# Kernel optimization log

Hardware: AMD Instinct MI355X
Metric: run time of the kernel (lower is better)

The kernel has to match this reference:

```python
import jax, jax.numpy as jnp
import numpy as np

B, T, IN_DIM = 32, 1024, 32
E, H, P = 256, 4, 32  # embed_dim, heads, max_patches
HD = E // H


def _lin(x, w, b):
    # torch nn.Linear: y = x @ W.T + b, W: [out, in]
    return jnp.einsum('...i,oi->...o', x, w) + b


def setup_inputs() -> dict:
    key = jax.random.key(0)
    ks = jax.random.split(key, 13)
    s = 0.02
    return {
        'x': jax.random.normal(ks[0], (B, T, IN_DIM), jnp.float32),
        'ip_w': jax.random.normal(ks[1], (E, IN_DIM), jnp.float32) * s,
        'ip_b': jnp.zeros((E,), jnp.float32),
        'in_proj_w': jax.random.normal(ks[2], (3 * E, E), jnp.float32) * s,
        'in_proj_b': jnp.zeros((3 * E,), jnp.float32),
        'out_w': jax.random.normal(ks[3], (E, E), jnp.float32) * s,
        'out_b': jnp.zeros((E,), jnp.float32),
        'bp_w1': jax.random.normal(ks[4], (32, E), jnp.float32) * s,
        'bp_b1': jnp.zeros((32,), jnp.float32),
        'bp_w2': jax.random.normal(ks[5], (1, 32), jnp.float32) * s,
        'bp_b2': jnp.zeros((1,), jnp.float32),
        'pr_w': jax.random.normal(ks[6], (E, E), jnp.float32) * s,
        'pr_b': jnp.zeros((E,), jnp.float32),
    }


def reference(x, ip_w, ip_b, in_proj_w, in_proj_b, out_w, out_b,
              bp_w1, bp_b1, bp_w2, bp_b2, pr_w, pr_b):
    # input projection
    h = _lin(x, ip_w, ip_b)  # [B,T,E]
    # MultiheadAttention (self-attn, batch_first, eval/no-dropout)
    qkv = _lin(h, in_proj_w, in_proj_b)  # [B,T,3E]
    q, k, v = jnp.split(qkv, 3, axis=-1)
    q = q.reshape(B, T, H, HD)
    k = k.reshape(B, T, H, HD)
    v = v.reshape(B, T, H, HD)
    scores = jnp.einsum('bqhd,bkhd->bhqk', q, k) / jnp.sqrt(jnp.float32(HD))
    attn = jax.nn.softmax(scores, axis=-1)
    ctx = jnp.einsum('bhqk,bkhd->bqhd', attn, v).reshape(B, T, E)
    attn_out = _lin(ctx, out_w, out_b)  # [B,T,E]
    # boundary scores
    bscore = jax.nn.sigmoid(_lin(jax.nn.relu(_lin(attn_out, bp_w1, bp_b1)), bp_w2, bp_b2))[..., 0]  # [B,T]
    cbp = jnp.cumsum(bscore, axis=1)
    cbp = cbp / (cbp[:, -1:] + 1e-6)
    pid = jnp.minimum(jnp.floor(cbp * P).astype(jnp.int32), P - 1)  # [B,T]
    # segment-mean pooling via scatter-add
    b_idx = jnp.broadcast_to(jnp.arange(B)[:, None], (B, T))
    pe = jnp.zeros((B, P, E), attn_out.dtype).at[b_idx, pid].add(attn_out)
    cnt = jnp.zeros((B, P), attn_out.dtype).at[b_idx, pid].add(1.0)
    pe = pe / jnp.clip(cnt, 1.0)[..., None]
    return _lin(pe, pr_w, pr_b)  # [B,P,E]
```

## Files before the change

### kernel.cpp

```cpp
#include <hip/hip_runtime.h>
#include <math.h>

constexpr int Bn  = 32;
constexpr int Tn  = 1024;
constexpr int INn = 32;
constexpr int En  = 256;
constexpr int Pn  = 32;

typedef short bf16x8 __attribute__((ext_vector_type(8)));
typedef float f32x4  __attribute__((ext_vector_type(4)));

__device__ __forceinline__ unsigned short f2bf(float f) {
    unsigned int b = __float_as_uint(f);
    b += 0x7FFF + ((b >> 16) & 1);
    return (unsigned short)(b >> 16);
}
__device__ __forceinline__ float bf2f(unsigned short h) {
    return __uint_as_float(((unsigned int)h) << 16);
}

__global__ __launch_bounds__(256) void k_prep(const float* __restrict__ ipw,
                                              const float* __restrict__ ipb,
                                              const float* __restrict__ inw,
                                              const float* __restrict__ inb,
                                              const float* __restrict__ outw,
                                              const float* __restrict__ w1,
                                              const float* __restrict__ x,
                                              unsigned short* __restrict__ Wcb,
                                              float* __restrict__ bc,
                                              unsigned short* __restrict__ Wb,
                                              unsigned short* __restrict__ w1h,
                                              unsigned short* __restrict__ w1l,
                                              unsigned short* __restrict__ xb) {
    int blk = blockIdx.x, tid = threadIdx.x;
    if (blk < 96) {
        int idx = blk * 256 + tid;
        int o = idx >> 5, i = idx & 31;
        const float* wr = inw + (size_t)o * En;
        float a0 = 0.f, a1 = 0.f;
        for (int e = 0; e < En; e += 2) {
            a0 += wr[e]     * ipw[(size_t)e * INn + i];
            a1 += wr[e + 1] * ipw[(size_t)(e + 1) * INn + i];
        }
        Wcb[(size_t)o * INn + i] = f2bf(a0 + a1);
    } else if (blk < 99) {
        int o = (blk - 96) * 256 + tid;
        const float* wr = inw + (size_t)o * En;
        float a = inb[o];
        for (int e = 0; e < En; ++e) a += wr[e] * ipb[e];
        bc[o] = a;
    } else if (blk < 163) {
        int idx = (blk - 99) * 256 + tid;
        float4 a = *(const float4*)(outw + (size_t)idx * 4);
        unsigned int u0 = f2bf(a.x) | ((unsigned int)f2bf(a.y) << 16);
        unsigned int u1 = f2bf(a.z) | ((unsigned int)f2bf(a.w) << 16);
        *(uint2*)(Wb + (size_t)idx * 4) = make_uint2(u0, u1);
    } else if (blk < 1187) {
        int idx = (blk - 163) * 256 + tid;
        float4 a = *(const float4*)(x + (size_t)idx * 4);
        unsigned int u0 = f2bf(a.x) | ((unsigned int)f2bf(a.y) << 16);
        unsigned int u1 = f2bf(a.z) | ((unsigned int)f2bf(a.w) << 16);
        *(uint2*)(xb + (size_t)idx * 4) = make_uint2(u0, u1);
    } else {
        int idx = (blk - 1187) * 256 + tid;
        float a = w1[idx];
        unsigned short h = f2bf(a);
        w1h[idx] = h;
        w1l[idx] = f2bf(a - bf2f(h));
    }
}

__global__ __launch_bounds__(256, 2) void k_qkv(const unsigned short* __restrict__ xb,
                                                const unsigned short* __restrict__ Wcb,
                                                const float* __restrict__ bc,
                                                unsigned short* __restrict__ Qb,
                                                unsigned short* __restrict__ Kb,
                                                unsigned short* __restrict__ Vt) {
    int tid = threadIdx.x;
    int wv = tid >> 6, lane = tid & 63;
    int cl = lane & 15, quad = lane >> 4;
    int m0 = blockIdx.x * 64;
    int b = m0 >> 10, tl0 = m0 & 1023;
    int n0w = wv * 192;
    f32x4 zero4 = {0.f, 0.f, 0.f, 0.f};

    bf16x8 wfrag[12]; float bv[12];
#pragma unroll
    for (int nt = 0; nt < 12; ++nt) {
        int col = n0w + nt * 16 + cl;
        wfrag[nt] = *(const bf16x8*)(Wcb + (size_t)col * 32 + quad * 8);
        bv[nt] = bc[col];
    }
#pragma unroll
    for (int mt = 0; mt < 4; ++mt) {
        bf16x8 af = *(const bf16x8*)(xb + (size_t)(m0 + mt * 16 + cl) * 32 + quad * 8);
        f32x4 acc[12];
#pragma unroll
        for (int nt = 0; nt < 12; ++nt)
            acc[nt] = __builtin_amdgcn_mfma_f32_16x16x32_bf16(af, wfrag[nt], zero4, 0, 0, 0);
        int tloc = tl0 + mt * 16 + quad * 4;
#pragma unroll
        for (int nt = 0; nt < 12; ++nt) {
            int col = n0w + nt * 16 + cl;
            int slot = col >> 8, c = col & 255;
            int h = c >> 6, d = c & 63;
            int bh = b * 4 + h;
            if (slot == 2) {
                unsigned int u0 = f2bf(acc[nt][0] + bv[nt]) |
                                  ((unsigned int)f2bf(acc[nt][1] + bv[nt]) << 16);
                unsigned int u1 = f2bf(acc[nt][2] + bv[nt]) |
                                  ((unsigned int)f2bf(acc[nt][3] + bv[nt]) << 16);
                *(uint2*)(Vt + ((size_t)bh * 64 + d) * 1024 + tloc) = make_uint2(u0, u1);
            } else {
                unsigned short* dst = (slot ? Kb : Qb) +
                                      ((size_t)bh * 1024 + tloc) * 64 + d;
#pragma unroll
                for (int r = 0; r < 4; ++r)
                    dst[(size_t)r * 64] = f2bf(acc[nt][r] + bv[nt]);
            }
        }
    }
}

__global__ __launch_bounds__(256, 2) void k_attn(const unsigned short* __restrict__ Qb,
                                                 const unsigned short* __restrict__ Kb,
                                                 const unsigned short* __restrict__ Vt,
                                                 unsigned short* __restrict__ Ctx) {
    __shared__ unsigned short Ks[64][72];
    __shared__ unsigned short Vs[64][72];
    __shared__ __align__(16) unsigned short Pl[4][4][16][40];
    int blk = blockIdx.x;
    int bh = blk & 127, qb = blk >> 7;
    int b = bh >> 2, h = bh & 3;
    int tid = threadIdx.x;
    int wv = tid >> 6, lane = tid & 63;
    int cl = lane & 15, quad = lane >> 4;
    int qbase = qb * 256 + wv * 64;

    f32x4 zero4 = {0.f, 0.f, 0.f, 0.f};
    bf16x8 qfrag[4][2];
#pragma unroll
    for (int tt = 0; tt < 4; ++tt)
#pragma unroll
        for (int ch = 0; ch < 2; ++ch)
            qfrag[tt][ch] = *(const bf16x8*)(Qb +
                ((size_t)bh * 1024 + qbase + tt * 16 + cl) * 64 + ch * 32 + quad * 8);
    f32x4 acc[4][4];
#pragma unroll
    for (int tt = 0; tt < 4; ++tt)
#pragma unroll
        for (int dt = 0; dt < 4; ++dt) acc[tt][dt] = zero4;
    float l[4] = {0.f, 0.f, 0.f, 0.f};

    const unsigned short* Kbase = Kb + (size_t)bh * 65536;
    const unsigned short* Vbase = Vt + (size_t)bh * 65536;

    for (int kt = 0; kt < 16; ++kt) {
#pragma unroll
        for (int r = 0; r < 2; ++r) {
            int idx = r * 256 + tid; int row = idx >> 3, c16 = idx & 7;
            *(uint4*)&Ks[row][c16 * 8] =
                *(const uint4*)(Kbase + (size_t)(kt * 64 + row) * 64 + c16 * 8);
            *(uint4*)&Vs[row][c16 * 8] =
                *(const uint4*)(Vbase + (size_t)row * 1024 + kt * 64 + c16 * 8);
        }
        __syncthreads();
#pragma unroll
        for (int c = 0; c < 2; ++c) {
            bf16x8 ka0 = *(const bf16x8*)&Ks[c * 32 + cl][quad * 8];
            bf16x8 ka1 = *(const bf16x8*)&Ks[c * 32 + cl][32 + quad * 8];
            bf16x8 kb0 = *(const bf16x8*)&Ks[c * 32 + 16 + cl][quad * 8];
            bf16x8 kb1 = *(const bf16x8*)&Ks[c * 32 + 16 + cl][32 + quad * 8];
            bf16x8 va[4];
#pragma unroll
            for (int dt = 0; dt < 4; ++dt)
                va[dt] = *(const bf16x8*)&Vs[dt * 16 + cl][c * 32 + quad * 8];
#pragma unroll
            for (int tt = 0; tt < 4; ++tt) {
                f32x4 s0 = __builtin_amdgcn_mfma_f32_16x16x32_bf16(ka0, qfrag[tt][0], zero4, 0, 0, 0);
                s0 = __builtin_amdgcn_mfma_f32_16x16x32_bf16(ka1, qfrag[tt][1], s0, 0, 0, 0);
                f32x4 s1 = __builtin_amdgcn_mfma_f32_16x16x32_bf16(kb0, qfrag[tt][0], zero4, 0, 0, 0);
                s1 = __builtin_amdgcn_mfma_f32_16x16x32_bf16(kb1, qfrag[tt][1], s1, 0, 0, 0);
                float p0 = __expf(0.125f * s0[0]), p1 = __expf(0.125f * s0[1]);
                float p2 = __expf(0.125f * s0[2]), p3 = __expf(0.125f * s0[3]);
                float p4 = __expf(0.125f * s1[0]), p5 = __expf(0.125f * s1[1]);
                float p6 = __expf(0.125f * s1[2]), p7 = __expf(0.125f * s1[3]);
                l[tt] += ((p0 + p1) + (p2 + p3)) + ((p4 + p5) + (p6 + p7));
                unsigned int w0 = f2bf(p0) | ((unsigned int)f2bf(p1) << 16);
                unsigned int w1 = f2bf(p2) | ((unsigned int)f2bf(p3) << 16);
                unsigned int w2 = f2bf(p4) | ((unsigned int)f2bf(p5) << 16);
                unsigned int w3 = f2bf(p6) | ((unsigned int)f2bf(p7) << 16);
                *(uint2*)&Pl[wv][tt][cl][quad * 4]      = make_uint2(w0, w1);
                *(uint2*)&Pl[wv][tt][cl][16 + quad * 4] = make_uint2(w2, w3);
            }
            asm volatile("s_waitcnt lgkmcnt(0)" ::: "memory");
#pragma unroll
            for (int tt = 0; tt < 4; ++tt) {
                bf16x8 pf = *(const bf16x8*)&Pl[wv][tt][cl][quad * 8];
#pragma unroll
                for (int dt = 0; dt < 4; ++dt)
                    acc[tt][dt] = __builtin_amdgcn_mfma_f32_16x16x32_bf16(pf, va[dt], acc[tt][dt], 0, 0, 0);
            }
        }
        __syncthreads();
    }
#pragma unroll
    for (int tt = 0; tt < 4; ++tt) {
        l[tt] += __shfl_xor(l[tt], 16);
        l[tt] += __shfl_xor(l[tt], 32);
        l[tt] = 1.f / l[tt];
    }
#pragma unroll
    for (int tt = 0; tt < 4; ++tt) {
#pragma unroll
        for (int r = 0; r < 4; ++r) {
            float rl = __shfl(l[tt], quad * 4 + r);
            size_t row = (size_t)(b * 1024 + qbase + tt * 16 + quad * 4 + r) * En;
#pragma unroll
            for (int dt = 0; dt < 4; ++dt)
                Ctx[row + h * 64 + dt * 16 + cl] = f2bf(acc[tt][dt][r] * rl);
        }
    }
}

__global__ __launch_bounds__(256) void k_out(const unsigned short* __restrict__ Ctx,
                                             const unsigned short* __restrict__ Wb,
                                             const float* __restrict__ bias,
                                             float* __restrict__ AO) {
    __shared__ unsigned short As[64][32];
    __shared__ unsigned short Bs[256][32];
    int tid = threadIdx.x;
    int wv = tid >> 6, lane = tid & 63;
    int cl = lane & 15, quad = lane >> 4;
    size_t m0 = (size_t)blockIdx.x * 64;

    f32x4 acc[4][4];
#pragma unroll
    for (int mt = 0; mt < 4; ++mt)
#pragma unroll
        for (int nt = 0; nt < 4; ++nt) acc[mt][nt] = {0.f, 0.f, 0.f, 0.f};

    for (int kt = 0; kt < 8; ++kt) {
        if (kt) __syncthreads();
        *(uint4*)&As[tid >> 2][(tid & 3) * 8] =
            *(const uint4*)(Ctx + (m0 + (tid >> 2)) * En + kt * 32 + (tid & 3) * 8);
#pragma unroll
        for (int j = 0; j < 4; ++j) {
            int lin = j * 256 + tid; int n = lin >> 2, c = lin & 3;
            *(uint4*)&Bs[n][c * 8] =
                *(const uint4*)(Wb + (size_t)n * En + kt * 32 + c * 8);
        }
        __syncthreads();
        bf16x8 af[4], bfr[4];
#pragma unroll
        for (int mt = 0; mt < 4; ++mt)
            af[mt] = *(const bf16x8*)&As[mt * 16 + cl][quad * 8];
#pragma unroll
        for (int nt = 0; nt < 4; ++nt)
            bfr[nt] = *(const bf16x8*)&Bs[wv * 64 + nt * 16 + cl][quad * 8];
#pragma unroll
        for (int mt = 0; mt < 4; ++mt)
#pragma unroll
            for (int nt = 0; nt < 4; ++nt)
                acc[mt][nt] = __builtin_amdgcn_mfma_f32_16x16x32_bf16(af[mt], bfr[nt], acc[mt][nt], 0, 0, 0);
    }
    float bv[4];
#pragma unroll
    for (int nt = 0; nt < 4; ++nt) bv[nt] = bias[wv * 64 + nt * 16 + cl];
#pragma unroll
    for (int mt = 0; mt < 4; ++mt)
#pragma unroll
        for (int nt = 0; nt < 4; ++nt)
#pragma unroll
            for (int r = 0; r < 4; ++r)
                AO[(m0 + mt * 16 + quad * 4 + r) * En + wv * 64 + nt * 16 + cl] =
                    acc[mt][nt][r] + bv[nt];
}

__global__ __launch_bounds__(256) void k_bscore(const float* __restrict__ AO,
                                                const unsigned short* __restrict__ w1h,
                                                const unsigned short* __restrict__ w1l,
                                                const float* __restrict__ b1,
                                                const float* __restrict__ w2,
                                                const float* __restrict__ b2,
                                                float* __restrict__ bsc) {
    __shared__ unsigned short Ah[128][72];
    __shared__ unsigned short Al[128][72];
    int tid = threadIdx.x;
    int wv = tid >> 6, lane = tid & 63;
    int cl = lane & 15, quad = lane >> 4;
    int m0 = blockIdx.x * 128;

    f32x4 acc[2][2];
#pragma unroll
    for (int mt = 0; mt < 2; ++mt)
#pragma unroll
        for (int nt = 0; nt < 2; ++nt) acc[mt][nt] = {0.f, 0.f, 0.f, 0.f};

    for (int kt = 0; kt < 4; ++kt) {
        if (kt) __syncthreads();
#pragma unroll
        for (int j = 0; j < 8; ++j) {
            int lin = j * 256 + tid; int row = lin >> 4, c4 = lin & 15;
            float4 a = *(const float4*)(AO + (size_t)(m0 + row) * En + kt * 64 + c4 * 4);
            unsigned short h0 = f2bf(a.x), h1v = f2bf(a.y), h2 = f2bf(a.z), h3 = f2bf(a.w);
            unsigned short l0 = f2bf(a.x - bf2f(h0)), l1v = f2bf(a.y - bf2f(h1v));
            unsigned short l2 = f2bf(a.z - bf2f(h2)), l3 = f2bf(a.w - bf2f(h3));
            *(uint2*)&Ah[row][c4 * 4] =
                make_uint2(h0 | ((unsigned int)h1v << 16), h2 | ((unsigned int)h3 << 16));
            *(uint2*)&Al[row][c4 * 4] =
                make_uint2(l0 | ((unsigned int)l1v << 16), l2 | ((unsigned int)l3 << 16));
        }
        __syncthreads();
#pragma unroll
        for (int ks = 0; ks < 2; ++ks) {
            bf16x8 bh_[2], bl_[2];
#pragma unroll
            for (int nt = 0; nt < 2; ++nt) {
                size_t off = (size_t)(nt * 16 + cl) * En + kt * 64 + ks * 32 + quad * 8;
                bh_[nt] = *(const bf16x8*)(w1h + off);
                bl_[nt] = *(const bf16x8*)(w1l + off);
            }
#pragma unroll
            for (int mt = 0; mt < 2; ++mt) {
                int row = wv * 32 + mt * 16 + cl;
                bf16x8 ah = *(const bf16x8*)&Ah[row][ks * 32 + quad * 8];
                bf16x8 al = *(const bf16x8*)&Al[row][ks * 32 + quad * 8];
#pragma unroll
                for (int nt = 0; nt < 2; ++nt) {
                    acc[mt][nt] = __builtin_amdgcn_mfma_f32_16x16x32_bf16(ah, bh_[nt], acc[mt][nt], 0, 0, 0);
                    acc[mt][nt] = __builtin_amdgcn_mfma_f32_16x16x32_bf16(ah, bl_[nt], acc[mt][nt], 0, 0, 0);
                    acc[mt][nt] = __builtin_amdgcn_mfma_f32_16x16x32_bf16(al, bh_[nt], acc[mt][nt], 0, 0, 0);
                }
            }
        }
    }
    float b1v[2], w2v[2];
#pragma unroll
    for (int nt = 0; nt < 2; ++nt) {
        b1v[nt] = b1[nt * 16 + cl];
        w2v[nt] = w2[nt * 16 + cl];
    }
    float b2v = b2[0];
#pragma unroll
    for (int mt = 0; mt < 2; ++mt) {
        f32x4 z;
#pragma unroll
        for (int r = 0; r < 4; ++r)
            z[r] = fmaxf(acc[mt][0][r] + b1v[0], 0.f) * w2v[0] +
                   fmaxf(acc[mt][1][r] + b1v[1], 0.f) * w2v[1];
#pragma unroll
        for (int d = 1; d < 16; d <<= 1)
#pragma unroll
            for (int r = 0; r < 4; ++r) z[r] += __shfl_xor(z[r], d);
        if (cl == 0) {
#pragma unroll
            for (int r = 0; r < 4; ++r)
                bsc[m0 + wv * 32 + mt * 16 + quad * 4 + r] =
                    1.f / (1.f + __expf(-(z[r] + b2v)));
        }
    }
}

__global__ __launch_bounds__(1024) void k_scan(const float* __restrict__ bsc,
                                               int* __restrict__ segs) {
    __shared__ float wsum[16];
    __shared__ float s_pre[1024];
    __shared__ float s_tot;
    int b = blockIdx.x, t = threadIdx.x;
    float x = bsc[b * Tn + t];
#pragma unroll
    for (int d = 1; d < 64; d <<= 1) {
        float y = __shfl_up(x, d);
        if ((t & 63) >= d) x += y;
    }
    int w = t >> 6;
    if ((t & 63) == 63) wsum[w] = x;
    __syncthreads();
    if (t == 0) {
        float s = 0.f;
        for (int i = 0; i < 16; ++i) { float tmp = wsum[i]; wsum[i] = s; s += tmp; }
        s_tot = s;
    }
    __syncthreads();
    float pre = x + wsum[w];
    s_pre[t] = pre;
    __syncthreads();
    float denom = s_tot + 1e-6f;
    float qv = pre / denom * 32.0f;
    int pid = min((int)floorf(qv), 31);
    int pidprev = -1;
    if (t > 0) {
        float qp = s_pre[t - 1] / denom * 32.0f;
        pidprev = min((int)floorf(qp), 31);
    }
    for (int p = pidprev + 1; p <= pid; ++p) segs[b * 33 + p] = t;
    if (t == 1023)
        for (int p = pid + 1; p <= 32; ++p) segs[b * 33 + p] = Tn;
}

__global__ __launch_bounds__(256) void k_pool_proj(const float* __restrict__ ao,
                                                   const int* __restrict__ segs,
                                                   const float* __restrict__ prw,
                                                   const float* __restrict__ prb,
                                                   float* __restrict__ out) {
    __shared__ float pes[En];
    int b = blockIdx.y, p = blockIdx.x;
    int s = segs[b * 33 + p];
    int e = segs[b * 33 + p + 1];
    int tid = threadIdx.x;
    float sum = 0.f;
    for (int t = s; t < e; ++t)
        sum += ao[((size_t)b * Tn + t) * En + tid];
    pes[tid] = sum / fmaxf((float)(e - s), 1.f);
    __syncthreads();
    float a0 = prb[tid], a1 = 0.f;
#pragma unroll
    for (int k = 0; k < En; k += 4) {
        float4 wv = *(const float4*)(prw + (size_t)tid * En + k);
        float4 pv = *(const float4*)&pes[k];
        a0 += wv.x * pv.x; a1 += wv.y * pv.y;
        a0 += wv.z * pv.z; a1 += wv.w * pv.w;
    }
    out[((size_t)b * Pn + p) * En + tid] = a0 + a1;
}

extern "C" void kernel_launch(void* const* d_in, const int* in_sizes, int n_in,
                              void* d_out, int out_size, void* d_ws, size_t ws_size,
                              hipStream_t stream) {
    const float* x    = (const float*)d_in[0];
    const float* ipw  = (const float*)d_in[1];
    const float* ipb  = (const float*)d_in[2];
    const float* inw  = (const float*)d_in[3];
    const float* inb  = (const float*)d_in[4];
    const float* outw = (const float*)d_in[5];
    const float* outb = (const float*)d_in[6];
    const float* bw1  = (const float*)d_in[7];
    const float* bb1  = (const float*)d_in[8];
    const float* bw2  = (const float*)d_in[9];
    const float* bb2  = (const float*)d_in[10];
    const float* prw  = (const float*)d_in[11];
    const float* prb  = (const float*)d_in[12];

    char* base = (char*)d_ws;
    unsigned short* Qb  = (unsigned short*)base;
    unsigned short* Kb  = Qb + (size_t)8388608;
    float*          AO  = (float*)base;
    unsigned short* Vt  = (unsigned short*)(base + (size_t)33554432);
    unsigned short* Ctx = (unsigned short*)(base + (size_t)50331648);
    unsigned short* xb  = (unsigned short*)(base + (size_t)67108864);
    unsigned short* Wcb = (unsigned short*)(base + (size_t)69206016);
    float*          bc  = (float*)(base + (size_t)69255168);
    unsigned short* Wb  = (unsigned short*)(base + (size_t)69258240);
    unsigned short* w1h = (unsigned short*)(base + (size_t)69389312);
    unsigned short* w1l = (unsigned short*)(base + (size_t)69405696);
    float*          bsc = (float*)(base + (size_t)69422080);
    int*           segs = (int*)(base + (size_t)69553152);

    k_prep<<<1219, 256, 0, stream>>>(ipw, ipb, inw, inb, outw, bw1, x,
                                     Wcb, bc, Wb, w1h, w1l, xb);
    k_qkv<<<512, 256, 0, stream>>>(xb, Wcb, bc, Qb, Kb, Vt);
    k_attn<<<512, 256, 0, stream>>>(Qb, Kb, Vt, Ctx);
    k_out<<<512, 256, 0, stream>>>(Ctx, Wb, outb, AO);
    k_bscore<<<256, 256, 0, stream>>>(AO, w1h, w1l, bb1, bw2, bb2, bsc);
    k_scan<<<32, 1024, 0, stream>>>(bsc, segs);
    k_pool_proj<<<dim3(32, 32), 256, 0, stream>>>(AO, segs, prw, prb,
                                                  (float*)d_out);
}
```

Before: 244.8 us.

## Split attention keys across two wave groups and fuse x conversion into QKV

The attention kernel now runs 512 threads per block. Two groups of four waves each process half of the key tiles for the same queries, then combine their partial context and row sums through shared memory before normalising. Separately, the fp32-to-bf16 conversion of x is moved from the prep kernel into the QKV kernel's operand load, which removes the intermediate xb buffer and its extra global round trip. Costs: the partial context is rounded to bf16 before the merge, shared memory grows, and there is an extra barrier at the end of attention.

New measurement: 517.3 us. 111% more time.

```diff
diff --git a/kernel.cpp b/kernel.cpp
--- a/kernel.cpp
+++ b/kernel.cpp
@@ -25,13 +25,11 @@
                                               const float* __restrict__ inb,
                                               const float* __restrict__ outw,
                                               const float* __restrict__ w1,
-                                              const float* __restrict__ x,
                                               unsigned short* __restrict__ Wcb,
                                               float* __restrict__ bc,
                                               unsigned short* __restrict__ Wb,
                                               unsigned short* __restrict__ w1h,
-                                              unsigned short* __restrict__ w1l,
-                                              unsigned short* __restrict__ xb) {
+                                              unsigned short* __restrict__ w1l) {
     int blk = blockIdx.x, tid = threadIdx.x;
     if (blk < 96) {
         int idx = blk * 256 + tid;
@@ -55,14 +53,8 @@
         unsigned int u0 = f2bf(a.x) | ((unsigned int)f2bf(a.y) << 16);
         unsigned int u1 = f2bf(a.z) | ((unsigned int)f2bf(a.w) << 16);
         *(uint2*)(Wb + (size_t)idx * 4) = make_uint2(u0, u1);
-    } else if (blk < 1187) {
+    } else {
         int idx = (blk - 163) * 256 + tid;
-        float4 a = *(const float4*)(x + (size_t)idx * 4);
-        unsigned int u0 = f2bf(a.x) | ((unsigned int)f2bf(a.y) << 16);
-        unsigned int u1 = f2bf(a.z) | ((unsigned int)f2bf(a.w) << 16);
-        *(uint2*)(xb + (size_t)idx * 4) = make_uint2(u0, u1);
-    } else {
-        int idx = (blk - 1187) * 256 + tid;
         float a = w1[idx];
         unsigned short h = f2bf(a);
         w1h[idx] = h;
@@ -70,7 +62,7 @@
     }
 }
 
-__global__ __launch_bounds__(256, 2) void k_qkv(const unsigned short* __restrict__ xb,
+__global__ __launch_bounds__(256, 2) void k_qkv(const float* __restrict__ x,
                                                 const unsigned short* __restrict__ Wcb,
                                                 const float* __restrict__ bc,
                                                 unsigned short* __restrict__ Qb,
@@ -93,7 +85,13 @@
     }
 #pragma unroll
     for (int mt = 0; mt < 4; ++mt) {
-        bf16x8 af = *(const bf16x8*)(xb + (size_t)(m0 + mt * 16 + cl) * 32 + quad * 8);
+        const float* xr = x + (size_t)(m0 + mt * 16 + cl) * 32 + quad * 8;
+        float4 xa = *(const float4*)xr, xc = *(const float4*)(xr + 4);
+        bf16x8 af;
+        af[0] = (short)f2bf(xa.x); af[1] = (short)f2bf(xa.y);
+        af[2] = (short)f2bf(xa.z); af[3] = (short)f2bf(xa.w);
+        af[4] = (short)f2bf(xc.x); af[5] = (short)f2bf(xc.y);
+        af[6] = (short)f2bf(xc.z); af[7] = (short)f2bf(xc.w);
         f32x4 acc[12];
 #pragma unroll
         for (int nt = 0; nt < 12; ++nt)
@@ -122,20 +120,27 @@
     }
 }
 
-__global__ __launch_bounds__(256, 2) void k_attn(const unsigned short* __restrict__ Qb,
+__global__ __launch_bounds__(512, 4) void k_attn(const unsigned short* __restrict__ Qb,
                                                  const unsigned short* __restrict__ Kb,
                                                  const unsigned short* __restrict__ Vt,
                                                  unsigned short* __restrict__ Ctx) {
-    __shared__ unsigned short Ks[64][72];
-    __shared__ unsigned short Vs[64][72];
-    __shared__ __align__(16) unsigned short Pl[4][4][16][40];
+    __shared__ __align__(16) unsigned short smem[38912];
+    unsigned short (*Ks)[64][72] = (unsigned short (*)[64][72])(smem);
+    unsigned short (*Vs)[64][72] = (unsigned short (*)[64][72])(smem + 9216);
+    unsigned short (*Pl)[4][16][40] = (unsigned short (*)[4][16][40])(smem + 18432);
+    unsigned short* Cl = smem;
+    float* Ll = (float*)(smem + 18432);
+
     int blk = blockIdx.x;
     int bh = blk & 127, qb = blk >> 7;
     int b = bh >> 2, h = bh & 3;
     int tid = threadIdx.x;
     int wv = tid >> 6, lane = tid & 63;
+    int qg = wv & 3, kk = wv >> 2;
+    int half = tid >> 8;
+    int t2 = tid & 255;
     int cl = lane & 15, quad = lane >> 4;
-    int qbase = qb * 256 + wv * 64;
+    int qbase = qb * 256 + qg * 64;
 
     f32x4 zero4 = {0.f, 0.f, 0.f, 0.f};
     bf16x8 qfrag[4][2];
@@ -155,26 +160,27 @@
     const unsigned short* Kbase = Kb + (size_t)bh * 65536;
     const unsigned short* Vbase = Vt + (size_t)bh * 65536;
 
-    for (int kt = 0; kt < 16; ++kt) {
+    for (int kt = 0; kt < 8; ++kt) {
+        int ktt = kt + 8 * half;
 #pragma unroll
         for (int r = 0; r < 2; ++r) {
-            int idx = r * 256 + tid; int row = idx >> 3, c16 = idx & 7;
-            *(uint4*)&Ks[row][c16 * 8] =
-                *(const uint4*)(Kbase + (size_t)(kt * 64 + row) * 64 + c16 * 8);
-            *(uint4*)&Vs[row][c16 * 8] =
-                *(const uint4*)(Vbase + (size_t)row * 1024 + kt * 64 + c16 * 8);
+            int idx = r * 256 + t2; int row = idx >> 3, c16 = idx & 7;
+            *(uint4*)&Ks[half][row][c16 * 8] =
+                *(const uint4*)(Kbase + (size_t)(ktt * 64 + row) * 64 + c16 * 8);
+            *(uint4*)&Vs[half][row][c16 * 8] =
+                *(const uint4*)(Vbase + (size_t)row * 1024 + ktt * 64 + c16 * 8);
         }
         __syncthreads();
 #pragma unroll
         for (int c = 0; c < 2; ++c) {
-            bf16x8 ka0 = *(const bf16x8*)&Ks[c * 32 + cl][quad * 8];
-            bf16x8 ka1 = *(const bf16x8*)&Ks[c * 32 + cl][32 + quad * 8];
-            bf16x8 kb0 = *(const bf16x8*)&Ks[c * 32 + 16 + cl][quad * 8];
-            bf16x8 kb1 = *(const bf16x8*)&Ks[c * 32 + 16 + cl][32 + quad * 8];
+            bf16x8 ka0 = *(const bf16x8*)&Ks[kk][c * 32 + cl][quad * 8];
+            bf16x8 ka1 = *(const bf16x8*)&Ks[kk][c * 32 + cl][32 + quad * 8];
+            bf16x8 kb0 = *(const bf16x8*)&Ks[kk][c * 32 + 16 + cl][quad * 8];
+            bf16x8 kb1 = *(const bf16x8*)&Ks[kk][c * 32 + 16 + cl][32 + quad * 8];
             bf16x8 va[4];
 #pragma unroll
             for (int dt = 0; dt < 4; ++dt)
-                va[dt] = *(const bf16x8*)&Vs[dt * 16 + cl][c * 32 + quad * 8];
+                va[dt] = *(const bf16x8*)&Vs[kk][dt * 16 + cl][c * 32 + quad * 8];
 #pragma unroll
             for (int tt = 0; tt < 4; ++tt) {
                 f32x4 s0 = __builtin_amdgcn_mfma_f32_16x16x32_bf16(ka0, qfrag[tt][0], zero4, 0, 0, 0);
@@ -208,17 +214,47 @@
     for (int tt = 0; tt < 4; ++tt) {
         l[tt] += __shfl_xor(l[tt], 16);
         l[tt] += __shfl_xor(l[tt], 32);
-        l[tt] = 1.f / l[tt];
-    }
-#pragma unroll
-    for (int tt = 0; tt < 4; ++tt) {
-#pragma unroll
-        for (int r = 0; r < 4; ++r) {
-            float rl = __shfl(l[tt], quad * 4 + r);
-            size_t row = (size_t)(b * 1024 + qbase + tt * 16 + quad * 4 + r) * En;
-#pragma unroll
-            for (int dt = 0; dt < 4; ++dt)
-                Ctx[row + h * 64 + dt * 16 + cl] = f2bf(acc[tt][dt][r] * rl);
+    }
+    if (kk == 1) {
+        unsigned short* dst = Cl + ((size_t)(qg * 64 + lane)) * 68;
+#pragma unroll
+        for (int tt = 0; tt < 4; ++tt)
+#pragma unroll
+            for (int dt = 0; dt < 4; ++dt) {
+                unsigned int u0 = f2bf(acc[tt][dt][0]) | ((unsigned int)f2bf(acc[tt][dt][1]) << 16);
+                unsigned int u1 = f2bf(acc[tt][dt][2]) | ((unsigned int)f2bf(acc[tt][dt][3]) << 16);
+                *(uint2*)(dst + (tt * 4 + dt) * 4) = make_uint2(u0, u1);
+            }
+        if (quad == 0) {
+#pragma unroll
+            for (int tt = 0; tt < 4; ++tt) Ll[qg * 64 + tt * 16 + cl] = l[tt];
+        }
+    }
+    __syncthreads();
+    if (kk == 0) {
+        const unsigned short* src = Cl + ((size_t)(qg * 64 + lane)) * 68;
+#pragma unroll
+        for (int tt = 0; tt < 4; ++tt) {
+#pragma unroll
+            for (int dt = 0; dt < 4; ++dt) {
+                uint2 u = *(const uint2*)(src + (tt * 4 + dt) * 4);
+                acc[tt][dt][0] += bf2f((unsigned short)(u.x & 0xffff));
+                acc[tt][dt][1] += bf2f((unsigned short)(u.x >> 16));
+                acc[tt][dt][2] += bf2f((unsigned short)(u.y & 0xffff));
+                acc[tt][dt][3] += bf2f((unsigned short)(u.y >> 16));
+            }
+            l[tt] = 1.f / (l[tt] + Ll[qg * 64 + tt * 16 + cl]);
+        }
+#pragma unroll
+        for (int tt = 0; tt < 4; ++tt) {
+#pragma unroll
+            for (int r = 0; r < 4; ++r) {
+                float rl = __shfl(l[tt], quad * 4 + r);
+                size_t row = (size_t)(b * 1024 + qbase + tt * 16 + quad * 4 + r) * En;
+#pragma unroll
+                for (int dt = 0; dt < 4; ++dt)
+                    Ctx[row + h * 64 + dt * 16 + cl] = f2bf(acc[tt][dt][r] * rl);
+            }
         }
     }
 }
@@ -448,7 +484,6 @@
     float*          AO  = (float*)base;
     unsigned short* Vt  = (unsigned short*)(base + (size_t)33554432);
     unsigned short* Ctx = (unsigned short*)(base + (size_t)50331648);
-    unsigned short* xb  = (unsigned short*)(base + (size_t)67108864);
     unsigned short* Wcb = (unsigned short*)(base + (size_t)69206016);
     float*          bc  = (float*)(base + (size_t)69255168);
     unsigned short* Wb  = (unsigned short*)(base + (size_t)69258240);
@@ -457,10 +492,10 @@
     float*          bsc = (float*)(base + (size_t)69422080);
     int*           segs = (int*)(base + (size_t)69553152);
 
-    k_prep<<<1219, 256, 0, stream>>>(ipw, ipb, inw, inb, outw, bw1, x,
-                                     Wcb, bc, Wb, w1h, w1l, xb);
-    k_qkv<<<512, 256, 0, stream>>>(xb, Wcb, bc, Qb, Kb, Vt);
-    k_attn<<<512, 256, 0, stream>>>(Qb, Kb, Vt, Ctx);
+    k_prep<<<195, 256, 0, stream>>>(ipw, ipb, inw, inb, outw, bw1,
+                                    Wcb, bc, Wb, w1h, w1l);
+    k_qkv<<<512, 256, 0, stream>>>(x, Wcb, bc, Qb, Kb, Vt);
+    k_attn<<<512, 512, 0, stream>>>(Qb, Kb, Vt, Ctx);
     k_out<<<512, 256, 0, stream>>>(Ctx, Wb, outb, AO);
     k_bscore<<<256, 256, 0, stream>>>(AO, w1h, w1l, bb1, bw2, bb2, bsc);
     k_scan<<<32, 1024, 0, stream>>>(bsc, segs);
```

## Split attention keys across two blocks and merge partials in output projection

Applied to the files above, without the earlier changes.

The attention kernel now splits each head's key range in half, launching four times as many blocks. Each block handles 128 queries over 512 keys, with 32 query rows per wave instead of 64. The unnormalized partial outputs and row sums are written separately, and the output-projection load combines the two halves and normalizes them. Separately, the bf16 conversion of x moves from the prep kernel into the QKV kernel's load. Both changes aim to raise occupancy and parallelism and to remove a conversion pass, at the cost of extra partial-output traffic. The merge sums bf16-rounded unnormalized partials, which stays correct only because the softmax has no running max.

Result: faster. 237.8 us (-2.9%).

```diff
diff --git a/kernel.cpp b/kernel.cpp
--- a/kernel.cpp
+++ b/kernel.cpp
@@ -25,13 +25,11 @@
                                               const float* __restrict__ inb,
                                               const float* __restrict__ outw,
                                               const float* __restrict__ w1,
-                                              const float* __restrict__ x,
                                               unsigned short* __restrict__ Wcb,
                                               float* __restrict__ bc,
                                               unsigned short* __restrict__ Wb,
                                               unsigned short* __restrict__ w1h,
-                                              unsigned short* __restrict__ w1l,
-                                              unsigned short* __restrict__ xb) {
+                                              unsigned short* __restrict__ w1l) {
     int blk = blockIdx.x, tid = threadIdx.x;
     if (blk < 96) {
         int idx = blk * 256 + tid;
@@ -55,14 +53,8 @@
         unsigned int u0 = f2bf(a.x) | ((unsigned int)f2bf(a.y) << 16);
         unsigned int u1 = f2bf(a.z) | ((unsigned int)f2bf(a.w) << 16);
         *(uint2*)(Wb + (size_t)idx * 4) = make_uint2(u0, u1);
-    } else if (blk < 1187) {
+    } else {
         int idx = (blk - 163) * 256 + tid;
-        float4 a = *(const float4*)(x + (size_t)idx * 4);
-        unsigned int u0 = f2bf(a.x) | ((unsigned int)f2bf(a.y) << 16);
-        unsigned int u1 = f2bf(a.z) | ((unsigned int)f2bf(a.w) << 16);
-        *(uint2*)(xb + (size_t)idx * 4) = make_uint2(u0, u1);
-    } else {
-        int idx = (blk - 1187) * 256 + tid;
         float a = w1[idx];
         unsigned short h = f2bf(a);
         w1h[idx] = h;
@@ -70,7 +62,7 @@
     }
 }
 
-__global__ __launch_bounds__(256, 2) void k_qkv(const unsigned short* __restrict__ xb,
+__global__ __launch_bounds__(256, 2) void k_qkv(const float* __restrict__ x,
                                                 const unsigned short* __restrict__ Wcb,
                                                 const float* __restrict__ bc,
                                                 unsigned short* __restrict__ Qb,
@@ -93,7 +85,13 @@
     }
 #pragma unroll
     for (int mt = 0; mt < 4; ++mt) {
-        bf16x8 af = *(const bf16x8*)(xb + (size_t)(m0 + mt * 16 + cl) * 32 + quad * 8);
+        const float* xr = x + (size_t)(m0 + mt * 16 + cl) * 32 + quad * 8;
+        float4 xa = *(const float4*)xr, xc = *(const float4*)(xr + 4);
+        bf16x8 af;
+        af[0] = (short)f2bf(xa.x); af[1] = (short)f2bf(xa.y);
+        af[2] = (short)f2bf(xa.z); af[3] = (short)f2bf(xa.w);
+        af[4] = (short)f2bf(xc.x); af[5] = (short)f2bf(xc.y);
+        af[6] = (short)f2bf(xc.z); af[7] = (short)f2bf(xc.w);
         f32x4 acc[12];
 #pragma unroll
         for (int nt = 0; nt < 12; ++nt)
@@ -122,47 +120,53 @@
     }
 }
 
-__global__ __launch_bounds__(256, 2) void k_attn(const unsigned short* __restrict__ Qb,
+__global__ __launch_bounds__(256, 4) void k_attn(const unsigned short* __restrict__ Qb,
                                                  const unsigned short* __restrict__ Kb,
                                                  const unsigned short* __restrict__ Vt,
-                                                 unsigned short* __restrict__ Ctx) {
+                                                 unsigned short* __restrict__ Po0,
+                                                 unsigned short* __restrict__ Po1,
+                                                 float* __restrict__ L0,
+                                                 float* __restrict__ L1) {
     __shared__ unsigned short Ks[64][72];
     __shared__ unsigned short Vs[64][72];
-    __shared__ __align__(16) unsigned short Pl[4][4][16][40];
+    __shared__ __align__(16) unsigned short Pl[4][2][16][40];
     int blk = blockIdx.x;
-    int bh = blk & 127, qb = blk >> 7;
+    int bh = blk & 127;
+    int r_ = blk >> 7;
+    int qb = r_ & 7, half = r_ >> 3;
     int b = bh >> 2, h = bh & 3;
     int tid = threadIdx.x;
     int wv = tid >> 6, lane = tid & 63;
     int cl = lane & 15, quad = lane >> 4;
-    int qbase = qb * 256 + wv * 64;
+    int qbase = qb * 128 + wv * 32;
 
     f32x4 zero4 = {0.f, 0.f, 0.f, 0.f};
-    bf16x8 qfrag[4][2];
-#pragma unroll
-    for (int tt = 0; tt < 4; ++tt)
+    bf16x8 qfrag[2][2];
+#pragma unroll
+    for (int tt = 0; tt < 2; ++tt)
 #pragma unroll
         for (int ch = 0; ch < 2; ++ch)
             qfrag[tt][ch] = *(const bf16x8*)(Qb +
                 ((size_t)bh * 1024 + qbase + tt * 16 + cl) * 64 + ch * 32 + quad * 8);
-    f32x4 acc[4][4];
-#pragma unroll
-    for (int tt = 0; tt < 4; ++tt)
+    f32x4 acc[2][4];
+#pragma unroll
+    for (int tt = 0; tt < 2; ++tt)
 #pragma unroll
         for (int dt = 0; dt < 4; ++dt) acc[tt][dt] = zero4;
-    float l[4] = {0.f, 0.f, 0.f, 0.f};
+    float l[2] = {0.f, 0.f};
 
     const unsigned short* Kbase = Kb + (size_t)bh * 65536;
     const unsigned short* Vbase = Vt + (size_t)bh * 65536;
 
-    for (int kt = 0; kt < 16; ++kt) {
+    for (int kt = 0; kt < 8; ++kt) {
+        int ktt = half * 8 + kt;
 #pragma unroll
         for (int r = 0; r < 2; ++r) {
             int idx = r * 256 + tid; int row = idx >> 3, c16 = idx & 7;
             *(uint4*)&Ks[row][c16 * 8] =
-                *(const uint4*)(Kbase + (size_t)(kt * 64 + row) * 64 + c16 * 8);
+                *(const uint4*)(Kbase + (size_t)(ktt * 64 + row) * 64 + c16 * 8);
             *(uint4*)&Vs[row][c16 * 8] =
-                *(const uint4*)(Vbase + (size_t)row * 1024 + kt * 64 + c16 * 8);
+                *(const uint4*)(Vbase + (size_t)row * 1024 + ktt * 64 + c16 * 8);
         }
         __syncthreads();
 #pragma unroll
@@ -176,7 +180,7 @@
             for (int dt = 0; dt < 4; ++dt)
                 va[dt] = *(const bf16x8*)&Vs[dt * 16 + cl][c * 32 + quad * 8];
 #pragma unroll
-            for (int tt = 0; tt < 4; ++tt) {
+            for (int tt = 0; tt < 2; ++tt) {
                 f32x4 s0 = __builtin_amdgcn_mfma_f32_16x16x32_bf16(ka0, qfrag[tt][0], zero4, 0, 0, 0);
                 s0 = __builtin_amdgcn_mfma_f32_16x16x32_bf16(ka1, qfrag[tt][1], s0, 0, 0, 0);
                 f32x4 s1 = __builtin_amdgcn_mfma_f32_16x16x32_bf16(kb0, qfrag[tt][0], zero4, 0, 0, 0);
@@ -195,7 +199,7 @@
             }
             asm volatile("s_waitcnt lgkmcnt(0)" ::: "memory");
 #pragma unroll
-            for (int tt = 0; tt < 4; ++tt) {
+            for (int tt = 0; tt < 2; ++tt) {
                 bf16x8 pf = *(const bf16x8*)&Pl[wv][tt][cl][quad * 8];
 #pragma unroll
                 for (int dt = 0; dt < 4; ++dt)
@@ -205,25 +209,33 @@
         __syncthreads();
     }
 #pragma unroll
-    for (int tt = 0; tt < 4; ++tt) {
+    for (int tt = 0; tt < 2; ++tt) {
         l[tt] += __shfl_xor(l[tt], 16);
         l[tt] += __shfl_xor(l[tt], 32);
-        l[tt] = 1.f / l[tt];
-    }
-#pragma unroll
-    for (int tt = 0; tt < 4; ++tt) {
+    }
+    unsigned short* Po = half ? Po1 : Po0;
+    float* Lp = half ? L1 : L0;
+#pragma unroll
+    for (int tt = 0; tt < 2; ++tt) {
 #pragma unroll
         for (int r = 0; r < 4; ++r) {
-            float rl = __shfl(l[tt], quad * 4 + r);
             size_t row = (size_t)(b * 1024 + qbase + tt * 16 + quad * 4 + r) * En;
 #pragma unroll
             for (int dt = 0; dt < 4; ++dt)
-                Ctx[row + h * 64 + dt * 16 + cl] = f2bf(acc[tt][dt][r] * rl);
-        }
-    }
-}
-
-__global__ __launch_bounds__(256) void k_out(const unsigned short* __restrict__ Ctx,
+                Po[row + h * 64 + dt * 16 + cl] = f2bf(acc[tt][dt][r]);
+        }
+    }
+    if (quad == 0) {
+#pragma unroll
+        for (int tt = 0; tt < 2; ++tt)
+            Lp[bh * 1024 + qbase + tt * 16 + cl] = l[tt];
+    }
+}
+
+__global__ __launch_bounds__(256) void k_out(const unsigned short* __restrict__ Po0,
+                                             const unsigned short* __restrict__ Po1,
+                                             const float* __restrict__ L0,
+                                             const float* __restrict__ L1,
                                              const unsigned short* __restrict__ Wb,
                                              const float* __restrict__ bias,
                                              float* __restrict__ AO) {
@@ -242,8 +254,27 @@
 
     for (int kt = 0; kt < 8; ++kt) {
         if (kt) __syncthreads();
-        *(uint4*)&As[tid >> 2][(tid & 3) * 8] =
-            *(const uint4*)(Ctx + (m0 + (tid >> 2)) * En + kt * 32 + (tid & 3) * 8);
+        {
+            int row = tid >> 2, c4 = tid & 3;
+            size_t g = (m0 + row) * En + kt * 32 + c4 * 8;
+            uint4 u0 = *(const uint4*)(Po0 + g);
+            uint4 u1 = *(const uint4*)(Po1 + g);
+            int gt = (int)(m0 + row);
+            int li = ((gt >> 10) * 4 + (kt >> 1)) * 1024 + (gt & 1023);
+            float linv = 1.f / (L0[li] + L1[li]);
+            unsigned int a0[4] = {u0.x, u0.y, u0.z, u0.w};
+            unsigned int a1[4] = {u1.x, u1.y, u1.z, u1.w};
+            unsigned int w[4];
+#pragma unroll
+            for (int j = 0; j < 4; ++j) {
+                float lo = (bf2f((unsigned short)(a0[j] & 0xffff)) +
+                            bf2f((unsigned short)(a1[j] & 0xffff))) * linv;
+                float hi = (bf2f((unsigned short)(a0[j] >> 16)) +
+                            bf2f((unsigned short)(a1[j] >> 16))) * linv;
+                w[j] = f2bf(lo) | ((unsigned int)f2bf(hi) << 16);
+            }
+            *(uint4*)&As[row][c4 * 8] = make_uint4(w[0], w[1], w[2], w[3]);
+        }
 #pragma unroll
         for (int j = 0; j < 4; ++j) {
             int lin = j * 256 + tid; int n = lin >> 2, c = lin & 3;
@@ -447,21 +478,23 @@
     unsigned short* Kb  = Qb + (size_t)8388608;
     float*          AO  = (float*)base;
     unsigned short* Vt  = (unsigned short*)(base + (size_t)33554432);
-    unsigned short* Ctx = (unsigned short*)(base + (size_t)50331648);
-    unsigned short* xb  = (unsigned short*)(base + (size_t)67108864);
-    unsigned short* Wcb = (unsigned short*)(base + (size_t)69206016);
-    float*          bc  = (float*)(base + (size_t)69255168);
-    unsigned short* Wb  = (unsigned short*)(base + (size_t)69258240);
-    unsigned short* w1h = (unsigned short*)(base + (size_t)69389312);
-    unsigned short* w1l = (unsigned short*)(base + (size_t)69405696);
-    float*          bsc = (float*)(base + (size_t)69422080);
-    int*           segs = (int*)(base + (size_t)69553152);
-
-    k_prep<<<1219, 256, 0, stream>>>(ipw, ipb, inw, inb, outw, bw1, x,
-                                     Wcb, bc, Wb, w1h, w1l, xb);
-    k_qkv<<<512, 256, 0, stream>>>(xb, Wcb, bc, Qb, Kb, Vt);
-    k_attn<<<512, 256, 0, stream>>>(Qb, Kb, Vt, Ctx);
-    k_out<<<512, 256, 0, stream>>>(Ctx, Wb, outb, AO);
+    unsigned short* Po0 = (unsigned short*)(base + (size_t)50331648);
+    unsigned short* Po1 = (unsigned short*)(base + (size_t)67108864);
+    unsigned short* Wcb = (unsigned short*)(base + (size_t)83886080);
+    float*          bc  = (float*)(base + (size_t)83935232);
+    unsigned short* Wb  = (unsigned short*)(base + (size_t)83938304);
+    unsigned short* w1h = (unsigned short*)(base + (size_t)84069376);
+    unsigned short* w1l = (unsigned short*)(base + (size_t)84085760);
+    float*          L0  = (float*)(base + (size_t)84102144);
+    float*          L1  = (float*)(base + (size_t)84626432);
+    float*          bsc = (float*)(base + (size_t)85150720);
+    int*           segs = (int*)(base + (size_t)85281792);
+
+    k_prep<<<195, 256, 0, stream>>>(ipw, ipb, inw, inb, outw, bw1,
+                                    Wcb, bc, Wb, w1h, w1l);
+    k_qkv<<<512, 256, 0, stream>>>(x, Wcb, bc, Qb, Kb, Vt);
+    k_attn<<<2048, 256, 0, stream>>>(Qb, Kb, Vt, Po0, Po1, L0, L1);
+    k_out<<<512, 256, 0, stream>>>(Po0, Po1, L0, L1, Wb, outb, AO);
     k_bscore<<<256, 256, 0, stream>>>(AO, w1h, w1l, bb1, bw2, bb2, bsc);
     k_scan<<<32, 1024, 0, stream>>>(bsc, segs);
     k_pool_proj<<<dim3(32, 32), 256, 0, stream>>>(AO, segs, prw, prb,
```
